# Kernel optimization log

Measured on AMD Instinct MI355X. Metric: run time of the kernel, lower is better.

Reference implementation:

```python
import jax, jax.numpy as jnp
import numpy as np

N = 50000          # nodes
E = 800000         # edges
F_IN, H, OUT = 512, 256, 2
BN_EPS = 1e-5


def setup_inputs() -> dict:
    key = jax.random.key(0)
    ks = jax.random.split(key, 10)
    x = jax.random.normal(ks[0], (N, F_IN), jnp.float32)
    edge_index = jax.random.randint(ks[1], (2, E), 0, N, dtype=jnp.int64)
    edge_weight = jax.random.uniform(ks[2], (E,), jnp.float32)

    def lin(k, fan_in, fan_out):
        return jax.random.normal(k, (fan_in, fan_out), jnp.float32) / np.sqrt(fan_in).astype(np.float32)

    W1, b1 = lin(ks[3], F_IN, H), jnp.zeros((H,), jnp.float32)
    W2, b2 = lin(ks[4], H, H), jnp.zeros((H,), jnp.float32)
    W3, b3 = lin(ks[5], H, OUT), jnp.zeros((OUT,), jnp.float32)
    # BatchNorm1d affine params + running stats (eval mode)
    g1, be1 = jnp.ones((H,), jnp.float32), jnp.zeros((H,), jnp.float32)
    m1 = 0.1 * jax.random.normal(ks[6], (H,), jnp.float32)
    v1 = jax.random.uniform(ks[7], (H,), jnp.float32, 0.5, 1.5)
    g2, be2 = jnp.ones((H,), jnp.float32), jnp.zeros((H,), jnp.float32)
    m2 = 0.1 * jax.random.normal(ks[8], (H,), jnp.float32)
    v2 = jax.random.uniform(ks[9], (H,), jnp.float32, 0.5, 1.5)
    return {"x": x, "edge_index": edge_index, "edge_weight": edge_weight,
            "W1": W1, "b1": b1, "g1": g1, "be1": be1, "m1": m1, "v1": v1,
            "W2": W2, "b2": b2, "g2": g2, "be2": be2, "m2": m2, "v2": v2,
            "W3": W3, "b3": b3}


def gcn_conv(x, row, col, w, W, b):
    # PyG GCNConv (eval): h = x @ W; out[col] += norm * h[row]; + b
    # row/col/w already include self-loops with weight 1.
    n = x.shape[0]
    h = x @ W                                      # [N, out]
    deg = jax.ops.segment_sum(w, col, num_segments=n)
    dinv = jnp.where(deg > 0, jax.lax.rsqrt(deg), 0.0)
    norm = dinv[row] * w * dinv[col]               # [E+N]
    out = jax.ops.segment_sum(h[row] * norm[:, None], col, num_segments=n)
    return out + b


def batchnorm_eval(x, g, be, m, v):
    return (x - m) * jax.lax.rsqrt(v + BN_EPS) * g + be


def reference(x, edge_index, edge_weight, W1, b1, g1, be1, m1, v1,
              W2, b2, g2, be2, m2, v2, W3, b3):
    n = x.shape[0]
    loops = jnp.arange(n, dtype=edge_index.dtype)
    row = jnp.concatenate([edge_index[0], loops])
    col = jnp.concatenate([edge_index[1], loops])
    w = jnp.concatenate([edge_weight, jnp.ones((n,), x.dtype)])

    h = jax.nn.relu(batchnorm_eval(gcn_conv(x, row, col, w, W1, b1), g1, be1, m1, v1))
    h = jax.nn.relu(batchnorm_eval(gcn_conv(h, row, col, w, W2, b2), g2, be2, m2, v2))
    return gcn_conv(h, row, col, w, W3, b3)
```

## Files before the change

kernel.cpp:

```cpp
#include <hip/hip_runtime.h>
#include <stdint.h>

#define F_IN 512
#define HF 256
#define OUT_F 2
#define BN_EPS 1e-5f
#define SCAN_B 256
#define LDSTR 36

typedef __attribute__((ext_vector_type(8))) short bf16x8;
typedef __attribute__((ext_vector_type(8))) unsigned short u16x8;
typedef __attribute__((ext_vector_type(4))) float f32x4;

__device__ inline float bf2f(unsigned short u) {
    union { float f; uint32_t i; } v; v.i = ((uint32_t)u) << 16; return v.f;
}
__device__ inline unsigned short f2bf(float f) {
    union { float f; uint32_t i; } v; v.f = f;
    uint32_t r = v.i + 0x7FFFu + ((v.i >> 16) & 1u);
    return (unsigned short)(r >> 16);
}

__global__ void prep_kernel(unsigned long long* __restrict__ packed,
                            const float* __restrict__ W1, unsigned short* __restrict__ W1t,
                            const float* __restrict__ W2, unsigned short* __restrict__ W2t,
                            unsigned short* __restrict__ bufa_pad,
                            int n, int pada) {
    int idx = blockIdx.x * blockDim.x + threadIdx.x;
    if (idx < n) { packed[idx] = 1ULL << 20; return; }
    int j = idx - n;
    if (j < F_IN * HF) {
        int nn = j >> 9, k = j & (F_IN - 1);
        W1t[j] = f2bf(W1[(size_t)k * HF + nn]);
        return;
    }
    j -= F_IN * HF;
    if (j < HF * HF) {
        int nn = j >> 8, k = j & (HF - 1);
        W2t[j] = f2bf(W2[(size_t)k * HF + nn]);
        return;
    }
    j -= HF * HF;
    if (j < pada) bufa_pad[j] = 0;
}

__global__ void count_kernel(const int* __restrict__ col,
                             const float* __restrict__ w,
                             unsigned long long* __restrict__ packed, int e) {
    int tid = blockIdx.x * blockDim.x + threadIdx.x;
    if (tid < e) {
        unsigned long long add = (1ULL << 40)
            | (unsigned long long)__float2uint_rn(w[tid] * 1048576.0f);
        atomicAdd(&packed[col[tid]], add);
    }
}

template<int AFP32>
__device__ inline bf16x8 load_a(const void* base, size_t elem_off) {
    if constexpr (AFP32) {
        const float* p = (const float*)base + elem_off;
        float4 f0 = *(const float4*)p;
        float4 f1 = *(const float4*)(p + 4);
        bf16x8 r;
        r[0] = (short)f2bf(f0.x); r[1] = (short)f2bf(f0.y);
        r[2] = (short)f2bf(f0.z); r[3] = (short)f2bf(f0.w);
        r[4] = (short)f2bf(f1.x); r[5] = (short)f2bf(f1.y);
        r[6] = (short)f2bf(f1.z); r[7] = (short)f2bf(f1.w);
        return r;
    } else {
        return *(const bf16x8*)((const unsigned short*)base + elem_off);
    }
}

template<int AFP32>
__global__ __launch_bounds__(256)
void gemm_kernel(const void* __restrict__ Av,
                 const unsigned short* __restrict__ Bt,
                 unsigned short* __restrict__ C, int K, int rowclamp) {
    __shared__ unsigned short As[2][128 * LDSTR];
    __shared__ unsigned short Bs[2][128 * LDSTR];
    const int tid  = threadIdx.x;
    const int lane = tid & 63;
    const int wv   = tid >> 6;
    const int wrow = wv >> 1, wcol = wv & 1;
    const int m0 = blockIdx.x * 128;
    const int n0 = blockIdx.y * 128;

    const int sr = tid >> 2;
    const int sc = (tid & 3) * 8;

    int ra0 = m0 + sr, ra1 = m0 + sr + 64;
    if (AFP32) {
        ra0 = ra0 < rowclamp ? ra0 : rowclamp - 1;
        ra1 = ra1 < rowclamp ? ra1 : rowclamp - 1;
    }
    const size_t offA0 = (size_t)ra0 * K + sc;
    const size_t offA1 = (size_t)ra1 * K + sc;

    const unsigned short* pb0 = Bt + (size_t)(n0 + sr) * K + sc;
    const unsigned short* pb1 = Bt + (size_t)(n0 + sr + 64) * K + sc;

    f32x4 zero4 = {0.0f, 0.0f, 0.0f, 0.0f};
    f32x4 acc[4][4];
    #pragma unroll
    for (int i = 0; i < 4; ++i)
        #pragma unroll
        for (int j = 0; j < 4; ++j) acc[i][j] = zero4;

    const int q8 = (lane >> 4) * 8;
    const int ml = lane & 15;

    bf16x8 va0 = load_a<AFP32>(Av, offA0);
    bf16x8 va1 = load_a<AFP32>(Av, offA1);
    bf16x8 vb0 = *(const bf16x8*)pb0;
    bf16x8 vb1 = *(const bf16x8*)pb1;

    const int nsteps = K >> 5;
    for (int s = 0; s < nsteps; ++s) {
        const int buf = s & 1;
        *(bf16x8*)&As[buf][sr * LDSTR + sc]        = va0;
        *(bf16x8*)&As[buf][(sr + 64) * LDSTR + sc] = va1;
        *(bf16x8*)&Bs[buf][sr * LDSTR + sc]        = vb0;
        *(bf16x8*)&Bs[buf][(sr + 64) * LDSTR + sc] = vb1;
        __syncthreads();
        if (s + 1 < nsteps) {
            int off = (s + 1) * 32;
            va0 = load_a<AFP32>(Av, offA0 + off);
            va1 = load_a<AFP32>(Av, offA1 + off);
            vb0 = *(const bf16x8*)(pb0 + off);
            vb1 = *(const bf16x8*)(pb1 + off);
        }
        bf16x8 af[4], bfr[4];
        #pragma unroll
        for (int i = 0; i < 4; ++i)
            af[i] = *(const bf16x8*)&As[buf][(wrow * 64 + i * 16 + ml) * LDSTR + q8];
        #pragma unroll
        for (int j = 0; j < 4; ++j)
            bfr[j] = *(const bf16x8*)&Bs[buf][(wcol * 64 + j * 16 + ml) * LDSTR + q8];
        #pragma unroll
        for (int i = 0; i < 4; ++i)
            #pragma unroll
            for (int j = 0; j < 4; ++j)
                acc[i][j] = __builtin_amdgcn_mfma_f32_16x16x32_bf16(af[i], bfr[j], acc[i][j], 0, 0, 0);
    }

    const int q4 = (lane >> 4) * 4;
    #pragma unroll
    for (int i = 0; i < 4; ++i) {
        #pragma unroll
        for (int j = 0; j < 4; ++j) {
            #pragma unroll
            for (int rg = 0; rg < 4; ++rg) {
                int r = m0 + wrow * 64 + i * 16 + q4 + rg;
                int c = n0 + wcol * 64 + j * 16 + ml;
                C[(size_t)r * HF + c] = f2bf(acc[i][j][rg]);
            }
        }
    }
}

__global__ void scan1_kernel(const unsigned long long* __restrict__ packed,
                             int* __restrict__ local, int* __restrict__ blocksum, int n) {
    __shared__ int tmp[SCAN_B];
    int i = blockIdx.x * SCAN_B + threadIdx.x;
    int v = (i < n) ? (int)(packed[i] >> 40) : 0;
    tmp[threadIdx.x] = v;
    __syncthreads();
    for (int off = 1; off < SCAN_B; off <<= 1) {
        int t = 0;
        if ((int)threadIdx.x >= off) t = tmp[threadIdx.x - off];
        __syncthreads();
        if ((int)threadIdx.x >= off) tmp[threadIdx.x] += t;
        __syncthreads();
    }
    if (i < n) local[i] = tmp[threadIdx.x] - v;
    if (threadIdx.x == SCAN_B - 1) blocksum[blockIdx.x] = tmp[SCAN_B - 1];
}

__global__ void scan3_dinv_kernel(int* __restrict__ csr_ptr, int* __restrict__ cursor,
                                  const int* __restrict__ blocksum,
                                  const unsigned long long* __restrict__ packed,
                                  float* __restrict__ dinv, int n, int e, int nb) {
    __shared__ int red[SCAN_B];
    int t = threadIdx.x;
    red[t] = (t < nb && t < (int)blockIdx.x) ? blocksum[t] : 0;
    __syncthreads();
    for (int off = SCAN_B / 2; off > 0; off >>= 1) {
        if (t < off) red[t] += red[t + off];
        __syncthreads();
    }
    int prefix = red[0];
    int i = blockIdx.x * SCAN_B + t;
    if (i < n) {
        int val = csr_ptr[i] + prefix;
        csr_ptr[i] = val;
        cursor[i] = val;
        float deg = (float)(packed[i] & 0xFFFFFFFFFFULL) * (1.0f / 1048576.0f);
        dinv[i] = rsqrtf(deg);
    }
    if (i == 0) csr_ptr[n] = e;
}

__global__ void fill_kernel(const int* __restrict__ row, const int* __restrict__ col,
                            const float* __restrict__ w, const float* __restrict__ dinv,
                            int* __restrict__ cursor, int2* __restrict__ csr_edge, int e) {
    int i = blockIdx.x * blockDim.x + threadIdx.x;
    if (i < e) {
        int r = row[i], c = col[i];
        int pos = atomicAdd(&cursor[c], 1);
        float nrm = dinv[r] * w[i] * dinv[c];
        csr_edge[pos] = make_int2(r, __float_as_int(nrm));
    }
}

#define AGBL 8
template<int FINAL>
__global__ void agg_kernel(const unsigned short* __restrict__ h,
                           const int* __restrict__ ptr,
                           const int2* __restrict__ edge,
                           const float* __restrict__ dinv,
                           const float* __restrict__ b, const float* __restrict__ g,
                           const float* __restrict__ be, const float* __restrict__ m,
                           const float* __restrict__ v,
                           unsigned short* __restrict__ out,
                           const float* __restrict__ W3, float* __restrict__ h3, int n) {
    int wid  = (blockIdx.x * blockDim.x + threadIdx.x) >> 6;
    int lane = threadIdx.x & 63;
    if (wid >= n) return;
    const int hi = lane >> 5;
    const int l  = lane & 31;
    const int fo = l * 8;

    int p0 = ptr[wid], p1 = ptr[wid + 1];
    int deg = p1 - p0;

    float a0 = 0.f, a1 = 0.f, a2 = 0.f, a3 = 0.f;
    float a4 = 0.f, a5 = 0.f, a6 = 0.f, a7 = 0.f;

    const int nb = deg & ~15;
    if (nb > 0) {
        int2 edc[AGBL];
        #pragma unroll
        for (int k = 0; k < AGBL; ++k) edc[k] = edge[p0 + 2 * k + hi];
        for (int t = 0; t < nb; t += 16) {
            u16x8 hv[AGBL];
            #pragma unroll
            for (int k = 0; k < AGBL; ++k)
                hv[k] = *(const u16x8*)(h + (size_t)(unsigned)edc[k].x * HF + fo);
            float wv[AGBL];
            #pragma unroll
            for (int k = 0; k < AGBL; ++k) wv[k] = __int_as_float(edc[k].y);
            if (t + 16 < nb) {
                #pragma unroll
                for (int k = 0; k < AGBL; ++k) edc[k] = edge[p0 + t + 16 + 2 * k + hi];
            }
            #pragma unroll
            for (int k = 0; k < AGBL; ++k) {
                a0 += wv[k] * bf2f(hv[k][0]);
                a1 += wv[k] * bf2f(hv[k][1]);
                a2 += wv[k] * bf2f(hv[k][2]);
                a3 += wv[k] * bf2f(hv[k][3]);
                a4 += wv[k] * bf2f(hv[k][4]);
                a5 += wv[k] * bf2f(hv[k][5]);
                a6 += wv[k] * bf2f(hv[k][6]);
                a7 += wv[k] * bf2f(hv[k][7]);
            }
        }
    }
    for (int t = nb; t < deg; t += 4) {
        int2 ed[2];
        float wv2[2];
        #pragma unroll
        for (int j = 0; j < 2; ++j) {
            int idx = t + 2 * j + hi;
            int cl = idx < deg ? idx : 0;
            ed[j] = edge[p0 + cl];
            wv2[j] = (idx < deg) ? __int_as_float(ed[j].y) : 0.0f;
        }
        u16x8 hv[2];
        #pragma unroll
        for (int j = 0; j < 2; ++j)
            hv[j] = *(const u16x8*)(h + (size_t)(unsigned)ed[j].x * HF + fo);
        #pragma unroll
        for (int j = 0; j < 2; ++j) {
            float nw = wv2[j];
            a0 += nw * bf2f(hv[j][0]);
            a1 += nw * bf2f(hv[j][1]);
            a2 += nw * bf2f(hv[j][2]);
            a3 += nw * bf2f(hv[j][3]);
            a4 += nw * bf2f(hv[j][4]);
            a5 += nw * bf2f(hv[j][5]);
            a6 += nw * bf2f(hv[j][6]);
            a7 += nw * bf2f(hv[j][7]);
        }
    }

    a0 += __shfl_xor(a0, 32, 64);
    a1 += __shfl_xor(a1, 32, 64);
    a2 += __shfl_xor(a2, 32, 64);
    a3 += __shfl_xor(a3, 32, 64);
    a4 += __shfl_xor(a4, 32, 64);
    a5 += __shfl_xor(a5, 32, 64);
    a6 += __shfl_xor(a6, 32, 64);
    a7 += __shfl_xor(a7, 32, 64);

    float s = dinv[wid];
    float sl = s * s;
    u16x8 hs = *(const u16x8*)(h + (size_t)wid * HF + fo);
    a0 += sl * bf2f(hs[0]);
    a1 += sl * bf2f(hs[1]);
    a2 += sl * bf2f(hs[2]);
    a3 += sl * bf2f(hs[3]);
    a4 += sl * bf2f(hs[4]);
    a5 += sl * bf2f(hs[5]);
    a6 += sl * bf2f(hs[6]);
    a7 += sl * bf2f(hs[7]);

    float4 bb0  = *(const float4*)(b + fo),      bb1  = *(const float4*)(b + fo + 4);
    float4 gg0  = *(const float4*)(g + fo),      gg1  = *(const float4*)(g + fo + 4);
    float4 bee0 = *(const float4*)(be + fo),     bee1 = *(const float4*)(be + fo + 4);
    float4 mm0  = *(const float4*)(m + fo),      mm1  = *(const float4*)(m + fo + 4);
    float4 vv0  = *(const float4*)(v + fo),      vv1  = *(const float4*)(v + fo + 4);
    float f0 = fmaxf((a0 + bb0.x - mm0.x) * rsqrtf(vv0.x + BN_EPS) * gg0.x + bee0.x, 0.f);
    float f1 = fmaxf((a1 + bb0.y - mm0.y) * rsqrtf(vv0.y + BN_EPS) * gg0.y + bee0.y, 0.f);
    float f2 = fmaxf((a2 + bb0.z - mm0.z) * rsqrtf(vv0.z + BN_EPS) * gg0.z + bee0.z, 0.f);
    float f3 = fmaxf((a3 + bb0.w - mm0.w) * rsqrtf(vv0.w + BN_EPS) * gg0.w + bee0.w, 0.f);
    float f4 = fmaxf((a4 + bb1.x - mm1.x) * rsqrtf(vv1.x + BN_EPS) * gg1.x + bee1.x, 0.f);
    float f5 = fmaxf((a5 + bb1.y - mm1.y) * rsqrtf(vv1.y + BN_EPS) * gg1.y + bee1.y, 0.f);
    float f6 = fmaxf((a6 + bb1.z - mm1.z) * rsqrtf(vv1.z + BN_EPS) * gg1.z + bee1.z, 0.f);
    float f7 = fmaxf((a7 + bb1.w - mm1.w) * rsqrtf(vv1.w + BN_EPS) * gg1.w + bee1.w, 0.f);

    if (!FINAL) {
        if (hi == 0) {
            u16x8 o;
            o[0] = f2bf(f0); o[1] = f2bf(f1); o[2] = f2bf(f2); o[3] = f2bf(f3);
            o[4] = f2bf(f4); o[5] = f2bf(f5); o[6] = f2bf(f6); o[7] = f2bf(f7);
            *(u16x8*)(out + (size_t)wid * HF + fo) = o;
        }
    } else {
        float4 w0 = *(const float4*)(W3 + fo * 2);
        float4 w1 = *(const float4*)(W3 + fo * 2 + 4);
        float4 w2 = *(const float4*)(W3 + fo * 2 + 8);
        float4 w3 = *(const float4*)(W3 + fo * 2 + 12);
        float s0 = f0 * w0.x + f1 * w0.z + f2 * w1.x + f3 * w1.z
                 + f4 * w2.x + f5 * w2.z + f6 * w3.x + f7 * w3.z;
        float s1 = f0 * w0.y + f1 * w0.w + f2 * w1.y + f3 * w1.w
                 + f4 * w2.y + f5 * w2.w + f6 * w3.y + f7 * w3.w;
        #pragma unroll
        for (int o = 16; o > 0; o >>= 1) {
            s0 += __shfl_xor(s0, o, 64);
            s1 += __shfl_xor(s1, o, 64);
        }
        if (lane == 0) {
            h3[wid * 2 + 0] = s0;
            h3[wid * 2 + 1] = s1;
        }
    }
}

__global__ void out_kernel(const float* __restrict__ h3,
                           const int* __restrict__ ptr, const int2* __restrict__ edge,
                           const float* __restrict__ dinv,
                           const float* __restrict__ b3, float* __restrict__ out, int n) {
    int i = blockIdx.x * blockDim.x + threadIdx.x;
    if (i >= n) return;
    int p0 = ptr[i], p1 = ptr[i + 1];
    float a0 = 0.f, a1 = 0.f;
    for (int p = p0; p < p1; p += 4) {
        #pragma unroll
        for (int k = 0; k < 4; ++k) {
            int idx = p + k < p1 ? p + k : p1 - 1;
            int2 e = edge[idx];
            float nw = (p + k < p1) ? __int_as_float(e.y) : 0.0f;
            float2 u = *(const float2*)(h3 + 2 * e.x);
            a0 += nw * u.x;
            a1 += nw * u.y;
        }
    }
    float s = dinv[i];
    float sl = s * s;
    out[2 * i + 0] = a0 + sl * h3[2 * i + 0] + b3[0];
    out[2 * i + 1] = a1 + sl * h3[2 * i + 1] + b3[1];
}

static inline char* align16(char* p) {
    return (char*)(((uintptr_t)p + 15) & ~(uintptr_t)15);
}

extern "C" void kernel_launch(void* const* d_in, const int* in_sizes, int n_in,
                              void* d_out, int out_size, void* d_ws, size_t ws_size,
                              hipStream_t stream) {
    const float* x   = (const float*)d_in[0];
    const int*   ei  = (const int*)d_in[1];
    const float* ew  = (const float*)d_in[2];
    const float* W1  = (const float*)d_in[3];
    const float* b1  = (const float*)d_in[4];
    const float* g1  = (const float*)d_in[5];
    const float* be1 = (const float*)d_in[6];
    const float* m1  = (const float*)d_in[7];
    const float* v1  = (const float*)d_in[8];
    const float* W2  = (const float*)d_in[9];
    const float* b2  = (const float*)d_in[10];
    const float* g2  = (const float*)d_in[11];
    const float* be2 = (const float*)d_in[12];
    const float* m2  = (const float*)d_in[13];
    const float* v2  = (const float*)d_in[14];
    const float* W3  = (const float*)d_in[15];
    const float* b3  = (const float*)d_in[16];

    const int N  = in_sizes[0] / F_IN;
    const int E  = in_sizes[2];
    const int MP = (N + 127) & ~127;
    const int* row = ei;
    const int* col = ei + E;

    char* wsb = (char*)d_ws;
    unsigned long long* packed = (unsigned long long*)wsb; wsb = align16(wsb + (size_t)N * 8);
    float* dinv     = (float*)wsb;          wsb = align16(wsb + (size_t)N * 4);
    int*   csr_ptr  = (int*)wsb;            wsb = align16(wsb + (size_t)(N + 1) * 4);
    int*   cursor   = (int*)wsb;            wsb = align16(wsb + (size_t)N * 4);
    int*   blocksum = (int*)wsb;            wsb = align16(wsb + (size_t)SCAN_B * 4);
    int2*  csr_edge = (int2*)wsb;           wsb = align16(wsb + (size_t)E * 8);
    unsigned short* W1t = (unsigned short*)wsb;  wsb = align16(wsb + (size_t)F_IN * HF * 2);
    unsigned short* W2t = (unsigned short*)wsb;  wsb = align16(wsb + (size_t)HF * HF * 2);
    unsigned short* bufh = (unsigned short*)wsb; wsb = align16(wsb + (size_t)MP * HF * 2);
    unsigned short* bufa = (unsigned short*)wsb; wsb = align16(wsb + (size_t)MP * HF * 2);
    float* h3 = (float*)wsb;                wsb = align16(wsb + (size_t)N * OUT_F * 4);
    float* outf = (float*)d_out;

    const int TB = 256;
    const int nscan = (N + SCAN_B - 1) / SCAN_B;
    const int pada = (MP - N) * HF;
    const int preptot = N + F_IN * HF + HF * HF + pada;

    prep_kernel<<<(preptot + TB - 1) / TB, TB, 0, stream>>>(
        packed, W1, W1t, W2, W2t, bufa + (size_t)N * HF, N, pada);

    count_kernel<<<(E + TB - 1) / TB, TB, 0, stream>>>(col, ew, packed, E);

    scan1_kernel<<<nscan, SCAN_B, 0, stream>>>(packed, csr_ptr, blocksum, N);
    scan3_dinv_kernel<<<nscan, SCAN_B, 0, stream>>>(csr_ptr, cursor, blocksum, packed, dinv, N, E, nscan);
    fill_kernel<<<(E + TB - 1) / TB, TB, 0, stream>>>(row, col, ew, dinv, cursor, csr_edge, E);

    dim3 ggrid(MP / 128, HF / 128);

    gemm_kernel<1><<<ggrid, TB, 0, stream>>>(x, W1t, bufh, F_IN, N);
    agg_kernel<0><<<((size_t)N * 64 + TB - 1) / TB, TB, 0, stream>>>(
        bufh, csr_ptr, csr_edge, dinv, b1, g1, be1, m1, v1, bufa, nullptr, nullptr, N);

    gemm_kernel<0><<<ggrid, TB, 0, stream>>>(bufa, W2t, bufh, HF, MP);
    agg_kernel<1><<<((size_t)N * 64 + TB - 1) / TB, TB, 0, stream>>>(
        bufh, csr_ptr, csr_edge, dinv, b2, g2, be2, m2, v2, nullptr, W3, h3, N);

    out_kernel<<<(N + TB - 1) / TB, TB, 0, stream>>>(h3, csr_ptr, csr_edge, dinv, b3, outf, N);
}
```

Measured before the change: 476.6 us.

## Retile GEMM to 64x256 full-width blocks and drop edge prefetch in aggregation

The GEMM block tile changes from 128x128 on a 2D grid to 64 rows by the full 256 output columns on a 1D grid. Each of the four waves now owns a 64-column slice and all waves share the same A tile. This reads each A row (x or the hidden activations) once instead of twice, at the cost of loading the whole B matrix per block and using more LDS. Separately, the aggregation kernel's software-prefetch of the next edge batch is removed and edges are loaded at the start of each iteration, which cuts register pressure but gives up latency hiding.

```diff
diff --git a/kernel.cpp b/kernel.cpp
--- a/kernel.cpp
+++ b/kernel.cpp
@@ -77,28 +77,24 @@
 void gemm_kernel(const void* __restrict__ Av,
                  const unsigned short* __restrict__ Bt,
                  unsigned short* __restrict__ C, int K, int rowclamp) {
-    __shared__ unsigned short As[2][128 * LDSTR];
-    __shared__ unsigned short Bs[2][128 * LDSTR];
+    __shared__ unsigned short As[2][64 * LDSTR];
+    __shared__ unsigned short Bs[2][256 * LDSTR];
     const int tid  = threadIdx.x;
     const int lane = tid & 63;
     const int wv   = tid >> 6;
-    const int wrow = wv >> 1, wcol = wv & 1;
-    const int m0 = blockIdx.x * 128;
-    const int n0 = blockIdx.y * 128;
+    const int m0 = blockIdx.x * 64;
 
     const int sr = tid >> 2;
     const int sc = (tid & 3) * 8;
 
-    int ra0 = m0 + sr, ra1 = m0 + sr + 64;
-    if (AFP32) {
-        ra0 = ra0 < rowclamp ? ra0 : rowclamp - 1;
-        ra1 = ra1 < rowclamp ? ra1 : rowclamp - 1;
-    }
-    const size_t offA0 = (size_t)ra0 * K + sc;
-    const size_t offA1 = (size_t)ra1 * K + sc;
-
-    const unsigned short* pb0 = Bt + (size_t)(n0 + sr) * K + sc;
-    const unsigned short* pb1 = Bt + (size_t)(n0 + sr + 64) * K + sc;
+    int ra = m0 + sr;
+    if (AFP32) ra = ra < rowclamp ? ra : rowclamp - 1;
+    const size_t offA = (size_t)ra * K + sc;
+
+    const unsigned short* pb0 = Bt + (size_t)(sr)       * K + sc;
+    const unsigned short* pb1 = Bt + (size_t)(sr + 64)  * K + sc;
+    const unsigned short* pb2 = Bt + (size_t)(sr + 128) * K + sc;
+    const unsigned short* pb3 = Bt + (size_t)(sr + 192) * K + sc;
 
     f32x4 zero4 = {0.0f, 0.0f, 0.0f, 0.0f};
     f32x4 acc[4][4];
@@ -110,33 +106,36 @@
     const int q8 = (lane >> 4) * 8;
     const int ml = lane & 15;
 
-    bf16x8 va0 = load_a<AFP32>(Av, offA0);
-    bf16x8 va1 = load_a<AFP32>(Av, offA1);
+    bf16x8 va  = load_a<AFP32>(Av, offA);
     bf16x8 vb0 = *(const bf16x8*)pb0;
     bf16x8 vb1 = *(const bf16x8*)pb1;
+    bf16x8 vb2 = *(const bf16x8*)pb2;
+    bf16x8 vb3 = *(const bf16x8*)pb3;
 
     const int nsteps = K >> 5;
     for (int s = 0; s < nsteps; ++s) {
         const int buf = s & 1;
-        *(bf16x8*)&As[buf][sr * LDSTR + sc]        = va0;
-        *(bf16x8*)&As[buf][(sr + 64) * LDSTR + sc] = va1;
-        *(bf16x8*)&Bs[buf][sr * LDSTR + sc]        = vb0;
-        *(bf16x8*)&Bs[buf][(sr + 64) * LDSTR + sc] = vb1;
+        *(bf16x8*)&As[buf][sr * LDSTR + sc]          = va;
+        *(bf16x8*)&Bs[buf][sr * LDSTR + sc]          = vb0;
+        *(bf16x8*)&Bs[buf][(sr + 64) * LDSTR + sc]   = vb1;
+        *(bf16x8*)&Bs[buf][(sr + 128) * LDSTR + sc]  = vb2;
+        *(bf16x8*)&Bs[buf][(sr + 192) * LDSTR + sc]  = vb3;
         __syncthreads();
         if (s + 1 < nsteps) {
             int off = (s + 1) * 32;
-            va0 = load_a<AFP32>(Av, offA0 + off);
-            va1 = load_a<AFP32>(Av, offA1 + off);
+            va  = load_a<AFP32>(Av, offA + off);
             vb0 = *(const bf16x8*)(pb0 + off);
             vb1 = *(const bf16x8*)(pb1 + off);
+            vb2 = *(const bf16x8*)(pb2 + off);
+            vb3 = *(const bf16x8*)(pb3 + off);
         }
         bf16x8 af[4], bfr[4];
         #pragma unroll
         for (int i = 0; i < 4; ++i)
-            af[i] = *(const bf16x8*)&As[buf][(wrow * 64 + i * 16 + ml) * LDSTR + q8];
+            af[i] = *(const bf16x8*)&As[buf][(i * 16 + ml) * LDSTR + q8];
         #pragma unroll
         for (int j = 0; j < 4; ++j)
-            bfr[j] = *(const bf16x8*)&Bs[buf][(wcol * 64 + j * 16 + ml) * LDSTR + q8];
+            bfr[j] = *(const bf16x8*)&Bs[buf][(wv * 64 + j * 16 + ml) * LDSTR + q8];
         #pragma unroll
         for (int i = 0; i < 4; ++i)
             #pragma unroll
@@ -151,8 +150,8 @@
         for (int j = 0; j < 4; ++j) {
             #pragma unroll
             for (int rg = 0; rg < 4; ++rg) {
-                int r = m0 + wrow * 64 + i * 16 + q4 + rg;
-                int c = n0 + wcol * 64 + j * 16 + ml;
+                int r = m0 + i * 16 + q4 + rg;
+                int c = wv * 64 + j * 16 + ml;
                 C[(size_t)r * HF + c] = f2bf(acc[i][j][rg]);
             }
         }
@@ -238,33 +237,25 @@
     float a4 = 0.f, a5 = 0.f, a6 = 0.f, a7 = 0.f;
 
     const int nb = deg & ~15;
-    if (nb > 0) {
-        int2 edc[AGBL];
-        #pragma unroll
-        for (int k = 0; k < AGBL; ++k) edc[k] = edge[p0 + 2 * k + hi];
-        for (int t = 0; t < nb; t += 16) {
-            u16x8 hv[AGBL];
-            #pragma unroll
-            for (int k = 0; k < AGBL; ++k)
-                hv[k] = *(const u16x8*)(h + (size_t)(unsigned)edc[k].x * HF + fo);
-            float wv[AGBL];
-            #pragma unroll
-            for (int k = 0; k < AGBL; ++k) wv[k] = __int_as_float(edc[k].y);
-            if (t + 16 < nb) {
-                #pragma unroll
-                for (int k = 0; k < AGBL; ++k) edc[k] = edge[p0 + t + 16 + 2 * k + hi];
-            }
-            #pragma unroll
-            for (int k = 0; k < AGBL; ++k) {
-                a0 += wv[k] * bf2f(hv[k][0]);
-                a1 += wv[k] * bf2f(hv[k][1]);
-                a2 += wv[k] * bf2f(hv[k][2]);
-                a3 += wv[k] * bf2f(hv[k][3]);
-                a4 += wv[k] * bf2f(hv[k][4]);
-                a5 += wv[k] * bf2f(hv[k][5]);
-                a6 += wv[k] * bf2f(hv[k][6]);
-                a7 += wv[k] * bf2f(hv[k][7]);
-            }
+    for (int t = 0; t < nb; t += 16) {
+        int2 ed[AGBL];
+        #pragma unroll
+        for (int k = 0; k < AGBL; ++k) ed[k] = edge[p0 + t + 2 * k + hi];
+        u16x8 hv[AGBL];
+        #pragma unroll
+        for (int k = 0; k < AGBL; ++k)
+            hv[k] = *(const u16x8*)(h + (size_t)(unsigned)ed[k].x * HF + fo);
+        #pragma unroll
+        for (int k = 0; k < AGBL; ++k) {
+            float nw = __int_as_float(ed[k].y);
+            a0 += nw * bf2f(hv[k][0]);
+            a1 += nw * bf2f(hv[k][1]);
+            a2 += nw * bf2f(hv[k][2]);
+            a3 += nw * bf2f(hv[k][3]);
+            a4 += nw * bf2f(hv[k][4]);
+            a5 += nw * bf2f(hv[k][5]);
+            a6 += nw * bf2f(hv[k][6]);
+            a7 += nw * bf2f(hv[k][7]);
         }
     }
     for (int t = nb; t < deg; t += 4) {
@@ -442,7 +433,7 @@
     scan3_dinv_kernel<<<nscan, SCAN_B, 0, stream>>>(csr_ptr, cursor, blocksum, packed, dinv, N, E, nscan);
     fill_kernel<<<(E + TB - 1) / TB, TB, 0, stream>>>(row, col, ew, dinv, cursor, csr_edge, E);
 
-    dim3 ggrid(MP / 128, HF / 128);
+    const int ggrid = MP / 64;
 
     gemm_kernel<1><<<ggrid, TB, 0, stream>>>(x, W1t, bufh, F_IN, N);
     agg_kernel<0><<<((size_t)N * 64 + TB - 1) / TB, TB, 0, stream>>>(
```

After: 475.5 us. Within noise of the previous version (-0.2%).
